# Kernel optimization log

Hardware: AMD Instinct MI355X
Metric: run time of the kernel (lower is better)

## Reference

```python
import jax, jax.numpy as jnp
import numpy as np

B, L, D = 1, 1024, 1024
NL = 4            # n_layers
N = 16            # d_state
DI = 2 * D        # d_inner (expand=2)
DTR = (D + 15) // 16  # dt_rank = ceil(d_model/16) = 64
K = 4             # depthwise conv kernel size
EPS = 1e-5


def setup_inputs() -> dict:
    key = jax.random.key(0)
    ks = jax.random.split(key, 8)
    s = lambda k, shp, sc: jax.random.normal(k, shp, jnp.float32) * sc
    x = s(ks[0], (B, L, D), 1.0)
    norm_w = jnp.ones((NL, D), jnp.float32)
    in_w = s(ks[1], (NL, 2 * DI, D), D ** -0.5)          # in_proj (no bias)
    conv_w = s(ks[2], (NL, DI, K), 0.5)                   # depthwise conv1d weight
    conv_b = s(ks[3], (NL, DI), 0.02)                     # conv1d bias
    xproj_w = s(ks[4], (NL, DTR + 2 * N, DI), DI ** -0.5) # x_proj (no bias)
    dt_w = s(ks[5], (NL, DI, DTR), DTR ** -0.5)           # dt_proj weight
    dt_b = jnp.full((NL, DI), 0.1, jnp.float32)           # dt_proj bias (positive-ish delta)
    A_log = jnp.log(jnp.tile(jnp.arange(1, N + 1, dtype=jnp.float32), (NL, DI, 1)))  # [NL, DI, N]
    D_skip = jnp.ones((NL, DI), jnp.float32)
    out_w = s(ks[6], (NL, D, DI), DI ** -0.5)             # out_proj (no bias)
    return dict(x=x, norm_w=norm_w, in_w=in_w, conv_w=conv_w, conv_b=conv_b,
                xproj_w=xproj_w, dt_w=dt_w, dt_b=dt_b, A_log=A_log,
                D_skip=D_skip, out_w=out_w)


def _rmsnorm(x, w):
    return x * jax.lax.rsqrt(jnp.mean(x * x, axis=-1, keepdims=True) + EPS) * w


def _causal_depthwise_conv(u, w, b):
    # u: [B, L, DI], w: [DI, K], b: [DI]; causal (left pad K-1)
    up = jnp.pad(u, ((0, 0), (K - 1, 0), (0, 0)))
    y = b
    for k in range(K):
        y = y + up[:, k:k + L, :] * w[:, k]
    return y


def _selective_scan(dA, dBu, C):
    # dA, dBu: [B, L, DI, N]; C: [B, L, N]
    def step(h, inp):
        a, bu, c = inp
        h = a * h + bu                       # [B, DI, N]
        y = jnp.einsum('bdn,bn->bd', h, c)   # [B, DI]
        return h, y
    h0 = jnp.zeros((dA.shape[0], DI, N), dA.dtype)
    _, ys = jax.lax.scan(step, h0, (dA.transpose(1, 0, 2, 3),
                                    dBu.transpose(1, 0, 2, 3),
                                    C.transpose(1, 0, 2)))
    return ys.transpose(1, 0, 2)             # [B, L, DI]


def _mamba_block(x, p):
    norm_w, in_w, conv_w, conv_b, xproj_w, dt_w, dt_b, A_log, D_skip, out_w = p
    xn = _rmsnorm(x, norm_w)
    xz = jnp.einsum('bld,ed->ble', xn, in_w)             # [B, L, 2*DI]
    u, z = jnp.split(xz, 2, axis=-1)
    u = jax.nn.silu(_causal_depthwise_conv(u, conv_w, conv_b))
    x_dbl = jnp.einsum('bld,ed->ble', u, xproj_w)        # [B, L, DTR+2N]
    dt_r, Bt, Ct = jnp.split(x_dbl, [DTR, DTR + N], axis=-1)
    delta = jax.nn.softplus(jnp.einsum('blr,dr->bld', dt_r, dt_w) + dt_b)  # [B, L, DI]
    A = -jnp.exp(A_log)                                  # [DI, N]
    dA = jnp.exp(delta[..., None] * A)                   # [B, L, DI, N]
    dBu = delta[..., None] * Bt[:, :, None, :] * u[..., None]
    y = _selective_scan(dA, dBu, Ct) + u * D_skip        # [B, L, DI]
    y = y * jax.nn.silu(z)
    return x + jnp.einsum('ble,de->bld', y, out_w)       # residual


def reference(x, norm_w, in_w, conv_w, conv_b, xproj_w, dt_w, dt_b, A_log, D_skip, out_w):
    params = (norm_w, in_w, conv_w, conv_b, xproj_w, dt_w, dt_b, A_log, D_skip, out_w)
    out, _ = jax.lax.scan(lambda h, p: (_mamba_block(h, p), None), x, params)
    return out
```

## Files before the change

### kernel.cpp

```cpp
#include <hip/hip_runtime.h>
#include <hip/hip_bf16.h>
#include <stdint.h>

#define L 1024
#define D 1024
#define NLAYER 4
#define NSTATE 16
#define DI 2048
#define DTR 64
#define KCONV 4
#define XD 96
#define NC 64
#define CT 16
#define KSPLIT 8

typedef __attribute__((ext_vector_type(8))) short short8;
typedef __attribute__((ext_vector_type(4))) float floatx4;

__device__ __forceinline__ float siluf(float x) { return x / (1.f + __expf(-x)); }

__device__ __forceinline__ unsigned short f2bf(float x) {
    __hip_bfloat16 b = __float2bfloat16(x);
    return *reinterpret_cast<unsigned short*>(&b);
}

#ifndef __has_builtin
#define __has_builtin(x) 0
#endif
#if __has_builtin(__builtin_amdgcn_global_load_lds)
#define HAVE_GLD 1
#define GLD(gp, lp) __builtin_amdgcn_global_load_lds(                                  \
    (const __attribute__((address_space(1))) void*)(gp),                               \
    (__attribute__((address_space(3))) void*)(lp), 16, 0, 0)
#endif

#define N_IN4  1048576
#define N_XP4  49152
#define N_DT4  32768
#define N_OUT4 524288
#define N_CVT4 (N_IN4 + N_XP4 + N_DT4 + N_OUT4)

__global__ __launch_bounds__(256) void cvt_layer_kernel(
    const float* __restrict__ in_w, const float* __restrict__ xp_w,
    const float* __restrict__ dt_w, const float* __restrict__ out_w,
    __hip_bfloat16* __restrict__ in_bf, __hip_bfloat16* __restrict__ xp_bf,
    __hip_bfloat16* __restrict__ dt_bf, __hip_bfloat16* __restrict__ out_bf) {
    int i = blockIdx.x * 256 + threadIdx.x;
    if (i >= N_CVT4) return;
    const float* src;
    __hip_bfloat16* dst;
    int off;
    if (i < N_IN4) { src = in_w; dst = in_bf; off = i; }
    else if (i < N_IN4 + N_XP4) { src = xp_w; dst = xp_bf; off = i - N_IN4; }
    else if (i < N_IN4 + N_XP4 + N_DT4) { src = dt_w; dst = dt_bf; off = i - N_IN4 - N_XP4; }
    else { src = out_w; dst = out_bf; off = i - N_IN4 - N_XP4 - N_DT4; }
    float4 v = ((const float4*)src)[off];
    ushort4 o;
    o.x = f2bf(v.x); o.y = f2bf(v.y); o.z = f2bf(v.z); o.w = f2bf(v.w);
    ((ushort4*)dst)[off] = o;
}

__global__ __launch_bounds__(256) void rmsnorm_kernel(const float* __restrict__ x,
                                                      const float* __restrict__ w,
                                                      __hip_bfloat16* __restrict__ out) {
    int row = blockIdx.x;
    const float* xr = x + (size_t)row * D;
    float v[4];
    float s = 0.f;
#pragma unroll
    for (int i = 0; i < 4; ++i) {
        v[i] = xr[threadIdx.x + i * 256];
        s += v[i] * v[i];
    }
#pragma unroll
    for (int off = 32; off > 0; off >>= 1) s += __shfl_xor(s, off, 64);
    __shared__ float red[4];
    int wave = threadIdx.x >> 6;
    if ((threadIdx.x & 63) == 0) red[wave] = s;
    __syncthreads();
    float tot = red[0] + red[1] + red[2] + red[3];
    float inv = rsqrtf(tot * (1.f / D) + 1e-5f);
#pragma unroll
    for (int i = 0; i < 4; ++i) {
        int c = threadIdx.x + i * 256;
        out[(size_t)row * D + c] = __float2bfloat16(v[i] * inv * w[c]);
    }
}

#define BM 128
#define BN 64
#define BK 32

template <int EPI>
__global__ __launch_bounds__(256, 2) void gemm_mfma(
    const __hip_bfloat16* __restrict__ A, int lda,
    const __hip_bfloat16* __restrict__ B, int ldb,
    float* __restrict__ C, int ldc, int Nvalid,
    int kchunk, long zstride,
    const float* __restrict__ bias, const float* __restrict__ resid) {
    __shared__ __align__(16) __hip_bfloat16 As[BM * BK];
    __shared__ __align__(16) __hip_bfloat16 Bs[BN * BK];
    int tid = threadIdx.x;
    int wave = tid >> 6, lane = tid & 63;
    int m0 = blockIdx.y * BM, n0 = blockIdx.x * BN;
    int k_lo = blockIdx.z * kchunk;
    int k_hi = k_lo + kchunk;
    C += (long)blockIdx.z * zstride;
    int wr = wave >> 1, wc = wave & 1;
    int srow = lane >> 2, scol = (lane & 3) * 8;
    int q = lane >> 4, r = lane & 15;

    floatx4 acc[4][2] = {};

    const __hip_bfloat16* gA = A + (long)(m0 + wave * 32 + srow) * lda + scol;
    const __hip_bfloat16* gB = B + (long)(n0 + wave * 16 + srow) * ldb + scol;
    __hip_bfloat16* lA0 = As + (wave * 32) * BK;
    __hip_bfloat16* lA1 = As + (wave * 32 + 16) * BK;
    __hip_bfloat16* lB  = Bs + (wave * 16) * BK;

    for (int k0 = k_lo; k0 < k_hi; k0 += BK) {
#ifdef HAVE_GLD
        GLD(gA + k0, lA0);
        GLD(gA + (long)16 * lda + k0, lA1);
        GLD(gB + k0, lB);
#else
        short8 a0 = *(const short8*)(gA + k0);
        short8 a1 = *(const short8*)(gA + (long)16 * lda + k0);
        short8 b0 = *(const short8*)(gB + k0);
        *(short8*)(lA0 + lane * 8) = a0;
        *(short8*)(lA1 + lane * 8) = a1;
        *(short8*)(lB + lane * 8) = b0;
#endif
        __syncthreads();
        const short* Ap = (const short*)As;
        const short* Bp = (const short*)Bs;
        short8 af[4], bfr[2];
#pragma unroll
        for (int i = 0; i < 4; ++i)
            af[i] = *(const short8*)(Ap + (wr * 64 + i * 16 + r) * BK + q * 8);
#pragma unroll
        for (int j = 0; j < 2; ++j)
            bfr[j] = *(const short8*)(Bp + (wc * 32 + j * 16 + r) * BK + q * 8);
#pragma unroll
        for (int i = 0; i < 4; ++i)
#pragma unroll
            for (int j = 0; j < 2; ++j)
                acc[i][j] = __builtin_amdgcn_mfma_f32_16x16x32_bf16(af[i], bfr[j], acc[i][j], 0, 0, 0);
        __syncthreads();
    }

#pragma unroll
    for (int i = 0; i < 4; ++i) {
        int mrow = m0 + wr * 64 + i * 16 + q * 4;
#pragma unroll
        for (int j = 0; j < 2; ++j) {
            int ncol = n0 + wc * 32 + j * 16 + r;
            if (ncol < Nvalid) {
#pragma unroll
                for (int rr = 0; rr < 4; ++rr) {
                    float v = acc[i][j][rr];
                    int m = mrow + rr;
                    if (EPI == 1) {
                        v += bias[ncol];
                        v = v > 20.f ? v : log1pf(__expf(v));
                    } else if (EPI == 2) {
                        v += resid[(long)m * ldc + ncol];
                    }
                    C[(long)m * ldc + ncol] = v;
                }
            }
        }
    }
}

__global__ __launch_bounds__(256) void conv_silu_kernel(const float* __restrict__ xz,
                                                        const float* __restrict__ cw,
                                                        const float* __restrict__ cb,
                                                        __hip_bfloat16* __restrict__ u) {
    int idx = blockIdx.x * 256 + threadIdx.x;
    int d = idx & (DI - 1);
    int t = idx >> 11;
    float acc = cb[d];
#pragma unroll
    for (int k = 0; k < KCONV; ++k) {
        int tk = t - (KCONV - 1) + k;
        if (tk >= 0) acc += xz[(size_t)tk * (2 * DI) + d] * cw[d * KCONV + k];
    }
    u[idx] = __float2bfloat16(siluf(acc));
}

__global__ __launch_bounds__(256) void xdbl_reduce_kernel(const float* __restrict__ part,
                                                          float* __restrict__ xdbl,
                                                          __hip_bfloat16* __restrict__ xdbl_bf) {
    int i = blockIdx.x * 256 + threadIdx.x;
    float s = 0.f;
#pragma unroll
    for (int sp = 0; sp < KSPLIT; ++sp) s += part[(long)sp * L * XD + i];
    xdbl[i] = s;
    xdbl_bf[i] = __float2bfloat16(s);
}

__global__ __launch_bounds__(256) void scanA_kernel(const float* __restrict__ delta,
                                                    const __hip_bfloat16* __restrict__ u,
                                                    const float* __restrict__ xdbl,
                                                    const float* __restrict__ Alog,
                                                    float* __restrict__ Ach,
                                                    float* __restrict__ Bch) {
    int d = blockIdx.x * 256 + threadIdx.x;
    int c = blockIdx.y;
    __shared__ __align__(16) float Bsh[CT * NSTATE];
    int tt0 = threadIdx.x >> 4, c0 = threadIdx.x & 15;
    Bsh[threadIdx.x] = xdbl[(size_t)(c * CT + tt0) * XD + DTR + c0];
    __syncthreads();

    float aval[NSTATE];
    const float4* Al4 = (const float4*)(Alog + (size_t)d * NSTATE);
#pragma unroll
    for (int n4 = 0; n4 < 4; ++n4) {
        float4 t = Al4[n4];
        aval[n4 * 4 + 0] = -__expf(t.x);
        aval[n4 * 4 + 1] = -__expf(t.y);
        aval[n4 * 4 + 2] = -__expf(t.z);
        aval[n4 * 4 + 3] = -__expf(t.w);
    }
    float h[NSTATE], ap[NSTATE];
#pragma unroll
    for (int n = 0; n < NSTATE; ++n) { h[n] = 0.f; ap[n] = 1.f; }

    for (int tt = 0; tt < CT; ++tt) {
        int t = c * CT + tt;
        float dl = delta[(size_t)t * DI + d];
        float uu = __bfloat162float(u[(size_t)t * DI + d]);
        float du = dl * uu;
        const float4* Bv = (const float4*)(Bsh + tt * NSTATE);
#pragma unroll
        for (int n4 = 0; n4 < 4; ++n4) {
            float4 b = Bv[n4];
            float bb[4] = {b.x, b.y, b.z, b.w};
#pragma unroll
            for (int k = 0; k < 4; ++k) {
                int n = n4 * 4 + k;
                float a = __expf(dl * aval[n]);
                h[n] = a * h[n] + du * bb[k];
                ap[n] *= a;
            }
        }
    }
    float4* Ao = (float4*)(Ach + ((size_t)c * DI + d) * NSTATE);
    float4* Bo = (float4*)(Bch + ((size_t)c * DI + d) * NSTATE);
#pragma unroll
    for (int n4 = 0; n4 < 4; ++n4) {
        Ao[n4] = make_float4(ap[n4 * 4], ap[n4 * 4 + 1], ap[n4 * 4 + 2], ap[n4 * 4 + 3]);
        Bo[n4] = make_float4(h[n4 * 4], h[n4 * 4 + 1], h[n4 * 4 + 2], h[n4 * 4 + 3]);
    }
}

__global__ __launch_bounds__(256) void scanB_kernel(float* __restrict__ Ach,
                                                    const float* __restrict__ Bch) {
    long i = blockIdx.x * 256 + threadIdx.x;
    const long S = (long)DI * NSTATE;
    float h = 0.f;
    for (int c = 0; c < NC; ++c) {
        float a = Ach[c * S + i];
        float b = Bch[c * S + i];
        Ach[c * S + i] = h;
        h = a * h + b;
    }
}

__global__ __launch_bounds__(256) void scanC_kernel(const float* __restrict__ delta,
                                                    const __hip_bfloat16* __restrict__ u,
                                                    const float* __restrict__ xdbl,
                                                    const float* __restrict__ Alog,
                                                    const float* __restrict__ Hin,
                                                    const float* __restrict__ xz,
                                                    const float* __restrict__ Dskip,
                                                    __hip_bfloat16* __restrict__ yg) {
    int d = blockIdx.x * 256 + threadIdx.x;
    int c = blockIdx.y;
    __shared__ __align__(16) float Bsh[CT * NSTATE];
    __shared__ __align__(16) float Csh[CT * NSTATE];
    int tt0 = threadIdx.x >> 4, c0 = threadIdx.x & 15;
    Bsh[threadIdx.x] = xdbl[(size_t)(c * CT + tt0) * XD + DTR + c0];
    Csh[threadIdx.x] = xdbl[(size_t)(c * CT + tt0) * XD + DTR + NSTATE + c0];
    __syncthreads();

    float aval[NSTATE];
    const float4* Al4 = (const float4*)(Alog + (size_t)d * NSTATE);
#pragma unroll
    for (int n4 = 0; n4 < 4; ++n4) {
        float4 t = Al4[n4];
        aval[n4 * 4 + 0] = -__expf(t.x);
        aval[n4 * 4 + 1] = -__expf(t.y);
        aval[n4 * 4 + 2] = -__expf(t.z);
        aval[n4 * 4 + 3] = -__expf(t.w);
    }
    float h[NSTATE];
    const float4* Hi = (const float4*)(Hin + ((size_t)c * DI + d) * NSTATE);
#pragma unroll
    for (int n4 = 0; n4 < 4; ++n4) {
        float4 t = Hi[n4];
        h[n4 * 4 + 0] = t.x; h[n4 * 4 + 1] = t.y; h[n4 * 4 + 2] = t.z; h[n4 * 4 + 3] = t.w;
    }
    float dsk = Dskip[d];

    for (int tt = 0; tt < CT; ++tt) {
        int t = c * CT + tt;
        float dl = delta[(size_t)t * DI + d];
        float uu = __bfloat162float(u[(size_t)t * DI + d]);
        float du = dl * uu;
        const float4* Bv = (const float4*)(Bsh + tt * NSTATE);
        const float4* Cv = (const float4*)(Csh + tt * NSTATE);
        float y = 0.f;
#pragma unroll
        for (int n4 = 0; n4 < 4; ++n4) {
            float4 b = Bv[n4];
            float4 cc = Cv[n4];
            float bb[4] = {b.x, b.y, b.z, b.w};
            float cv[4] = {cc.x, cc.y, cc.z, cc.w};
#pragma unroll
            for (int k = 0; k < 4; ++k) {
                int n = n4 * 4 + k;
                float a = __expf(dl * aval[n]);
                h[n] = a * h[n] + du * bb[k];
                y += h[n] * cv[k];
            }
        }
        float z = xz[(size_t)t * (2 * DI) + DI + d];
        yg[(size_t)t * DI + d] = __float2bfloat16((y + uu * dsk) * siluf(z));
    }
}

extern "C" void kernel_launch(void* const* d_in, const int* in_sizes, int n_in,
                              void* d_out, int out_size, void* d_ws, size_t ws_size,
                              hipStream_t stream) {
    const float* x      = (const float*)d_in[0];
    const float* norm_w = (const float*)d_in[1];
    const float* in_w   = (const float*)d_in[2];
    const float* conv_w = (const float*)d_in[3];
    const float* conv_b = (const float*)d_in[4];
    const float* xproj_w= (const float*)d_in[5];
    const float* dt_w   = (const float*)d_in[6];
    const float* dt_b   = (const float*)d_in[7];
    const float* A_log  = (const float*)d_in[8];
    const float* D_skip = (const float*)d_in[9];
    const float* out_w  = (const float*)d_in[10];
    float* out = (float*)d_out;

    uint8_t* wp = (uint8_t*)d_ws;
    auto alloc = [&](size_t bytes) {
        uint8_t* p = wp;
        wp += (bytes + 255) & ~(size_t)255;
        return p;
    };
    __hip_bfloat16* w_in_bf  = (__hip_bfloat16*)alloc((size_t)4096 * 1024 * 2);
    __hip_bfloat16* w_xp_bf  = (__hip_bfloat16*)alloc((size_t)128 * 2048 * 2);
    __hip_bfloat16* w_dt_bf  = (__hip_bfloat16*)alloc((size_t)2048 * 64 * 2);
    __hip_bfloat16* w_out_bf = (__hip_bfloat16*)alloc((size_t)1024 * 2048 * 2);
    __hip_bfloat16* xn_bf    = (__hip_bfloat16*)alloc((size_t)L * D * 2);
    float*          xz       = (float*)alloc((size_t)L * 2 * DI * 4);
    __hip_bfloat16* u_bf     = (__hip_bfloat16*)alloc((size_t)L * DI * 2);
    float*          xdbl     = (float*)alloc((size_t)L * XD * 4);
    __hip_bfloat16* xdbl_bf  = (__hip_bfloat16*)alloc((size_t)L * XD * 2);
    float*          part     = (float*)alloc((size_t)KSPLIT * L * XD * 4);
    float*          delta    = (float*)alloc((size_t)L * DI * 4);
    __hip_bfloat16* yg_bf    = (__hip_bfloat16*)alloc((size_t)L * DI * 2);
    float*          Ach      = (float*)alloc((size_t)NC * DI * NSTATE * 4);
    float*          Bch      = (float*)alloc((size_t)NC * DI * NSTATE * 4);

    for (int l = 0; l < NLAYER; ++l) {
        const float* xin = (l == 0) ? x : out;

        cvt_layer_kernel<<<(N_CVT4 + 255) / 256, 256, 0, stream>>>(
            in_w + (size_t)l * 4096 * 1024, xproj_w + (size_t)l * 96 * 2048,
            dt_w + (size_t)l * 2048 * 64, out_w + (size_t)l * 1024 * 2048,
            w_in_bf, w_xp_bf, w_dt_bf, w_out_bf);

        rmsnorm_kernel<<<L, 256, 0, stream>>>(xin, norm_w + (size_t)l * D, xn_bf);

        gemm_mfma<0><<<dim3(4096 / BN, L / BM, 1), 256, 0, stream>>>(
            xn_bf, D, w_in_bf, D, xz, 4096, 4096, D, 0, nullptr, nullptr);

        conv_silu_kernel<<<L * DI / 256, 256, 0, stream>>>(
            xz, conv_w + (size_t)l * DI * KCONV, conv_b + (size_t)l * DI, u_bf);

        gemm_mfma<0><<<dim3(2, L / BM, KSPLIT), 256, 0, stream>>>(
            u_bf, DI, w_xp_bf, DI, part, XD, XD, DI / KSPLIT, (long)L * XD, nullptr, nullptr);
        xdbl_reduce_kernel<<<(L * XD) / 256, 256, 0, stream>>>(part, xdbl, xdbl_bf);

        gemm_mfma<1><<<dim3(2048 / BN, L / BM, 1), 256, 0, stream>>>(
            xdbl_bf, XD, w_dt_bf, DTR, delta, DI, DI, DTR, 0,
            dt_b + (size_t)l * DI, nullptr);

        scanA_kernel<<<dim3(DI / 256, NC), 256, 0, stream>>>(
            delta, u_bf, xdbl, A_log + (size_t)l * DI * NSTATE, Ach, Bch);
        scanB_kernel<<<(DI * NSTATE) / 256, 256, 0, stream>>>(Ach, Bch);
        scanC_kernel<<<dim3(DI / 256, NC), 256, 0, stream>>>(
            delta, u_bf, xdbl, A_log + (size_t)l * DI * NSTATE, Ach, xz,
            D_skip + (size_t)l * DI, yg_bf);

        gemm_mfma<2><<<dim3(1024 / BN, L / BM, 1), 256, 0, stream>>>(
            yg_bf, DI, w_out_bf, DI, out, D, D, DI, 0, nullptr, xin);
    }
}
```

Baseline: 682.5 us.

## Fuse weight bf16 conversion into register-pipelined GEMMs and fuse residual with next RMSNorm

Drops the per-layer weight conversion kernel. The GEMMs now load fp32 weights directly, pack them to bf16 in registers, and use a register-prefetch pipeline (DIST=4) with double-buffered LDS and one barrier per k-step. The out-proj GEMM is split-K by two, and its reduction kernel also adds the residual and computes the next layer's RMSNorm. The x_proj output is split into a bf16 dt part and a compact fp32 B/C buffer for the scan. This trades the extra conversion pass and launches for twice the weight-read bandwidth inside the GEMMs and higher register pressure.

```diff
diff --git a/kernel.cpp b/kernel.cpp
--- a/kernel.cpp
+++ b/kernel.cpp
@@ -13,6 +13,8 @@
 #define NC 64
 #define CT 16
 #define KSPLIT 8
+#define BK 32
+#define DIST 4
 
 typedef __attribute__((ext_vector_type(8))) short short8;
 typedef __attribute__((ext_vector_type(4))) float floatx4;
@@ -24,41 +26,16 @@
     return *reinterpret_cast<unsigned short*>(&b);
 }
 
-#ifndef __has_builtin
-#define __has_builtin(x) 0
-#endif
-#if __has_builtin(__builtin_amdgcn_global_load_lds)
-#define HAVE_GLD 1
-#define GLD(gp, lp) __builtin_amdgcn_global_load_lds(                                  \
-    (const __attribute__((address_space(1))) void*)(gp),                               \
-    (__attribute__((address_space(3))) void*)(lp), 16, 0, 0)
-#endif
-
-#define N_IN4  1048576
-#define N_XP4  49152
-#define N_DT4  32768
-#define N_OUT4 524288
-#define N_CVT4 (N_IN4 + N_XP4 + N_DT4 + N_OUT4)
-
-__global__ __launch_bounds__(256) void cvt_layer_kernel(
-    const float* __restrict__ in_w, const float* __restrict__ xp_w,
-    const float* __restrict__ dt_w, const float* __restrict__ out_w,
-    __hip_bfloat16* __restrict__ in_bf, __hip_bfloat16* __restrict__ xp_bf,
-    __hip_bfloat16* __restrict__ dt_bf, __hip_bfloat16* __restrict__ out_bf) {
-    int i = blockIdx.x * 256 + threadIdx.x;
-    if (i >= N_CVT4) return;
-    const float* src;
-    __hip_bfloat16* dst;
-    int off;
-    if (i < N_IN4) { src = in_w; dst = in_bf; off = i; }
-    else if (i < N_IN4 + N_XP4) { src = xp_w; dst = xp_bf; off = i - N_IN4; }
-    else if (i < N_IN4 + N_XP4 + N_DT4) { src = dt_w; dst = dt_bf; off = i - N_IN4 - N_XP4; }
-    else { src = out_w; dst = out_bf; off = i - N_IN4 - N_XP4 - N_DT4; }
-    float4 v = ((const float4*)src)[off];
-    ushort4 o;
-    o.x = f2bf(v.x); o.y = f2bf(v.y); o.z = f2bf(v.z); o.w = f2bf(v.w);
-    ((ushort4*)dst)[off] = o;
-}
+__device__ __forceinline__ short8 pack8(floatx4 a, floatx4 b) {
+    short8 o;
+    o[0] = (short)f2bf(a.x); o[1] = (short)f2bf(a.y);
+    o[2] = (short)f2bf(a.z); o[3] = (short)f2bf(a.w);
+    o[4] = (short)f2bf(b.x); o[5] = (short)f2bf(b.y);
+    o[6] = (short)f2bf(b.z); o[7] = (short)f2bf(b.w);
+    return o;
+}
+
+#define BARRIER_NODRAIN() asm volatile("s_waitcnt lgkmcnt(0)\n\ts_barrier" ::: "memory")
 
 __global__ __launch_bounds__(256) void rmsnorm_kernel(const float* __restrict__ x,
                                                       const float* __restrict__ w,
@@ -87,24 +64,18 @@
     }
 }
 
-#define BM 128
-#define BN 64
-#define BK 32
-
-template <int EPI>
-__global__ __launch_bounds__(256, 2) void gemm_mfma(
+template <int EPI, int ITERS>
+__global__ __launch_bounds__(256, 2) void gemm_pipe(
     const __hip_bfloat16* __restrict__ A, int lda,
-    const __hip_bfloat16* __restrict__ B, int ldb,
+    const float* __restrict__ Bw, int ldb, int Brows,
     float* __restrict__ C, int ldc, int Nvalid,
-    int kchunk, long zstride,
-    const float* __restrict__ bias, const float* __restrict__ resid) {
-    __shared__ __align__(16) __hip_bfloat16 As[BM * BK];
-    __shared__ __align__(16) __hip_bfloat16 Bs[BN * BK];
+    long zstride, const float* __restrict__ bias) {
+    __shared__ __align__(16) __hip_bfloat16 As[2][128 * BK];
+    __shared__ __align__(16) __hip_bfloat16 Bs[2][64 * BK];
     int tid = threadIdx.x;
     int wave = tid >> 6, lane = tid & 63;
-    int m0 = blockIdx.y * BM, n0 = blockIdx.x * BN;
-    int k_lo = blockIdx.z * kchunk;
-    int k_hi = k_lo + kchunk;
+    int m0 = blockIdx.y * 128, n0 = blockIdx.x * 64;
+    int k_base = blockIdx.z * (ITERS * BK);
     C += (long)blockIdx.z * zstride;
     int wr = wave >> 1, wc = wave & 1;
     int srow = lane >> 2, scol = (lane & 3) * 8;
@@ -112,28 +83,44 @@
 
     floatx4 acc[4][2] = {};
 
-    const __hip_bfloat16* gA = A + (long)(m0 + wave * 32 + srow) * lda + scol;
-    const __hip_bfloat16* gB = B + (long)(n0 + wave * 16 + srow) * ldb + scol;
-    __hip_bfloat16* lA0 = As + (wave * 32) * BK;
-    __hip_bfloat16* lA1 = As + (wave * 32 + 16) * BK;
-    __hip_bfloat16* lB  = Bs + (wave * 16) * BK;
-
-    for (int k0 = k_lo; k0 < k_hi; k0 += BK) {
-#ifdef HAVE_GLD
-        GLD(gA + k0, lA0);
-        GLD(gA + (long)16 * lda + k0, lA1);
-        GLD(gB + k0, lB);
-#else
-        short8 a0 = *(const short8*)(gA + k0);
-        short8 a1 = *(const short8*)(gA + (long)16 * lda + k0);
-        short8 b0 = *(const short8*)(gB + k0);
-        *(short8*)(lA0 + lane * 8) = a0;
-        *(short8*)(lA1 + lane * 8) = a1;
-        *(short8*)(lB + lane * 8) = b0;
-#endif
-        __syncthreads();
-        const short* Ap = (const short*)As;
-        const short* Bp = (const short*)Bs;
+    const __hip_bfloat16* gA0 = A + (long)(m0 + wave * 32 + srow) * lda + scol + k_base;
+    const __hip_bfloat16* gA1 = gA0 + (long)16 * lda;
+    int bn = n0 + wave * 16 + srow;
+    const float* gB = Bw + (long)bn * ldb + scol + k_base;
+    bool bok = bn < Brows;
+
+    short8 qa0[DIST], qa1[DIST];
+    floatx4 qb0[DIST] = {}, qb1[DIST] = {};
+
+    auto ld = [&](int j) {
+        int k0 = j * BK;
+        int s = j & (DIST - 1);
+        qa0[s] = *(const short8*)(gA0 + k0);
+        qa1[s] = *(const short8*)(gA1 + k0);
+        if (bok) {
+            qb0[s] = *(const floatx4*)(gB + k0);
+            qb1[s] = *(const floatx4*)(gB + k0 + 4);
+        }
+    };
+    auto wrstage = [&](int j) {
+        int p = j & 1, s = j & (DIST - 1);
+        *(short8*)(&As[p][(wave * 32 + srow) * BK + scol]) = qa0[s];
+        *(short8*)(&As[p][(wave * 32 + 16 + srow) * BK + scol]) = qa1[s];
+        *(short8*)(&Bs[p][(wave * 16 + srow) * BK + scol]) = pack8(qb0[s], qb1[s]);
+    };
+
+#pragma unroll
+    for (int j = 0; j < DIST; ++j)
+        if (j < ITERS) ld(j);
+    wrstage(0);
+
+#pragma unroll
+    for (int k = 0; k < ITERS; ++k) {
+        BARRIER_NODRAIN();
+        if (k + DIST < ITERS) ld(k + DIST);
+        if (k + 1 < ITERS) wrstage(k + 1);
+        const short* Ap = (const short*)As[k & 1];
+        const short* Bp = (const short*)Bs[k & 1];
         short8 af[4], bfr[2];
 #pragma unroll
         for (int i = 0; i < 4; ++i)
@@ -146,7 +133,6 @@
 #pragma unroll
             for (int j = 0; j < 2; ++j)
                 acc[i][j] = __builtin_amdgcn_mfma_f32_16x16x32_bf16(af[i], bfr[j], acc[i][j], 0, 0, 0);
-        __syncthreads();
     }
 
 #pragma unroll
@@ -163,12 +149,45 @@
                     if (EPI == 1) {
                         v += bias[ncol];
                         v = v > 20.f ? v : log1pf(__expf(v));
-                    } else if (EPI == 2) {
-                        v += resid[(long)m * ldc + ncol];
                     }
                     C[(long)m * ldc + ncol] = v;
                 }
             }
+        }
+    }
+}
+
+template <bool NORM>
+__global__ __launch_bounds__(256) void reduce2_kernel(const float* __restrict__ part2,
+                                                      const float* __restrict__ xin,
+                                                      const float* __restrict__ nw,
+                                                      float* __restrict__ out,
+                                                      __hip_bfloat16* __restrict__ xn) {
+    int row = blockIdx.x;
+    const float* p0 = part2 + (size_t)row * D;
+    const float* p1 = p0 + (size_t)L * D;
+    const float* xr = xin + (size_t)row * D;
+    float v[4];
+    float ss = 0.f;
+#pragma unroll
+    for (int i = 0; i < 4; ++i) {
+        int c = threadIdx.x + i * 256;
+        v[i] = p0[c] + p1[c] + xr[c];
+        out[(size_t)row * D + c] = v[i];
+        ss += v[i] * v[i];
+    }
+    if (NORM) {
+#pragma unroll
+        for (int off = 32; off > 0; off >>= 1) ss += __shfl_xor(ss, off, 64);
+        __shared__ float red[4];
+        int wave = threadIdx.x >> 6;
+        if ((threadIdx.x & 63) == 0) red[wave] = ss;
+        __syncthreads();
+        float inv = rsqrtf((red[0] + red[1] + red[2] + red[3]) * (1.f / D) + 1e-5f);
+#pragma unroll
+        for (int i = 0; i < 4; ++i) {
+            int c = threadIdx.x + i * 256;
+            xn[(size_t)row * D + c] = __float2bfloat16(v[i] * inv * nw[c]);
         }
     }
 }
@@ -189,20 +208,21 @@
     u[idx] = __float2bfloat16(siluf(acc));
 }
 
-__global__ __launch_bounds__(256) void xdbl_reduce_kernel(const float* __restrict__ part,
-                                                          float* __restrict__ xdbl,
-                                                          __hip_bfloat16* __restrict__ xdbl_bf) {
+__global__ __launch_bounds__(256) void xred_kernel(const float* __restrict__ part,
+                                                   __hip_bfloat16* __restrict__ xdbl_bf,
+                                                   float* __restrict__ xdblBC) {
     int i = blockIdx.x * 256 + threadIdx.x;
+    int t = i / XD, col = i - t * XD;
     float s = 0.f;
 #pragma unroll
-    for (int sp = 0; sp < KSPLIT; ++sp) s += part[(long)sp * L * XD + i];
-    xdbl[i] = s;
-    xdbl_bf[i] = __float2bfloat16(s);
+    for (int sp = 0; sp < KSPLIT; ++sp) s += part[(size_t)sp * L * XD + i];
+    if (col < DTR) xdbl_bf[(size_t)t * DTR + col] = __float2bfloat16(s);
+    else xdblBC[(size_t)t * 32 + (col - DTR)] = s;
 }
 
 __global__ __launch_bounds__(256) void scanA_kernel(const float* __restrict__ delta,
                                                     const __hip_bfloat16* __restrict__ u,
-                                                    const float* __restrict__ xdbl,
+                                                    const float* __restrict__ xdblBC,
                                                     const float* __restrict__ Alog,
                                                     float* __restrict__ Ach,
                                                     float* __restrict__ Bch) {
@@ -210,7 +230,7 @@
     int c = blockIdx.y;
     __shared__ __align__(16) float Bsh[CT * NSTATE];
     int tt0 = threadIdx.x >> 4, c0 = threadIdx.x & 15;
-    Bsh[threadIdx.x] = xdbl[(size_t)(c * CT + tt0) * XD + DTR + c0];
+    Bsh[threadIdx.x] = xdblBC[(size_t)(c * CT + tt0) * 32 + c0];
     __syncthreads();
 
     float aval[NSTATE];
@@ -270,7 +290,7 @@
 
 __global__ __launch_bounds__(256) void scanC_kernel(const float* __restrict__ delta,
                                                     const __hip_bfloat16* __restrict__ u,
-                                                    const float* __restrict__ xdbl,
+                                                    const float* __restrict__ xdblBC,
                                                     const float* __restrict__ Alog,
                                                     const float* __restrict__ Hin,
                                                     const float* __restrict__ xz,
@@ -281,8 +301,8 @@
     __shared__ __align__(16) float Bsh[CT * NSTATE];
     __shared__ __align__(16) float Csh[CT * NSTATE];
     int tt0 = threadIdx.x >> 4, c0 = threadIdx.x & 15;
-    Bsh[threadIdx.x] = xdbl[(size_t)(c * CT + tt0) * XD + DTR + c0];
-    Csh[threadIdx.x] = xdbl[(size_t)(c * CT + tt0) * XD + DTR + NSTATE + c0];
+    Bsh[threadIdx.x] = xdblBC[(size_t)(c * CT + tt0) * 32 + c0];
+    Csh[threadIdx.x] = xdblBC[(size_t)(c * CT + tt0) * 32 + 16 + c0];
     __syncthreads();
 
     float aval[NSTATE];
@@ -353,53 +373,55 @@
         wp += (bytes + 255) & ~(size_t)255;
         return p;
     };
-    __hip_bfloat16* w_in_bf  = (__hip_bfloat16*)alloc((size_t)4096 * 1024 * 2);
-    __hip_bfloat16* w_xp_bf  = (__hip_bfloat16*)alloc((size_t)128 * 2048 * 2);
-    __hip_bfloat16* w_dt_bf  = (__hip_bfloat16*)alloc((size_t)2048 * 64 * 2);
-    __hip_bfloat16* w_out_bf = (__hip_bfloat16*)alloc((size_t)1024 * 2048 * 2);
-    __hip_bfloat16* xn_bf    = (__hip_bfloat16*)alloc((size_t)L * D * 2);
-    float*          xz       = (float*)alloc((size_t)L * 2 * DI * 4);
-    __hip_bfloat16* u_bf     = (__hip_bfloat16*)alloc((size_t)L * DI * 2);
-    float*          xdbl     = (float*)alloc((size_t)L * XD * 4);
-    __hip_bfloat16* xdbl_bf  = (__hip_bfloat16*)alloc((size_t)L * XD * 2);
-    float*          part     = (float*)alloc((size_t)KSPLIT * L * XD * 4);
-    float*          delta    = (float*)alloc((size_t)L * DI * 4);
-    __hip_bfloat16* yg_bf    = (__hip_bfloat16*)alloc((size_t)L * DI * 2);
-    float*          Ach      = (float*)alloc((size_t)NC * DI * NSTATE * 4);
-    float*          Bch      = (float*)alloc((size_t)NC * DI * NSTATE * 4);
+    __hip_bfloat16* xn_bf   = (__hip_bfloat16*)alloc((size_t)L * D * 2);
+    float*          xz      = (float*)alloc((size_t)L * 2 * DI * 4);
+    __hip_bfloat16* u_bf    = (__hip_bfloat16*)alloc((size_t)L * DI * 2);
+    float*          part    = (float*)alloc((size_t)KSPLIT * L * XD * 4);
+    __hip_bfloat16* xdbl_bf = (__hip_bfloat16*)alloc((size_t)L * DTR * 2);
+    float*          xdblBC  = (float*)alloc((size_t)L * 32 * 4);
+    float*          delta   = (float*)alloc((size_t)L * DI * 4);
+    __hip_bfloat16* yg_bf   = (__hip_bfloat16*)alloc((size_t)L * DI * 2);
+    float*          part2   = (float*)alloc((size_t)2 * L * D * 4);
+    float*          Ach     = (float*)alloc((size_t)NC * DI * NSTATE * 4);
+    float*          Bch     = (float*)alloc((size_t)NC * DI * NSTATE * 4);
+
+    rmsnorm_kernel<<<L, 256, 0, stream>>>(x, norm_w, xn_bf);
 
     for (int l = 0; l < NLAYER; ++l) {
         const float* xin = (l == 0) ? x : out;
 
-        cvt_layer_kernel<<<(N_CVT4 + 255) / 256, 256, 0, stream>>>(
-            in_w + (size_t)l * 4096 * 1024, xproj_w + (size_t)l * 96 * 2048,
-            dt_w + (size_t)l * 2048 * 64, out_w + (size_t)l * 1024 * 2048,
-            w_in_bf, w_xp_bf, w_dt_bf, w_out_bf);
-
-        rmsnorm_kernel<<<L, 256, 0, stream>>>(xin, norm_w + (size_t)l * D, xn_bf);
-
-        gemm_mfma<0><<<dim3(4096 / BN, L / BM, 1), 256, 0, stream>>>(
-            xn_bf, D, w_in_bf, D, xz, 4096, 4096, D, 0, nullptr, nullptr);
+        gemm_pipe<0, 32><<<dim3(4096 / 64, L / 128, 1), 256, 0, stream>>>(
+            xn_bf, D, in_w + (size_t)l * 4096 * 1024, D, 4096,
+            xz, 4096, 4096, 0, nullptr);
 
         conv_silu_kernel<<<L * DI / 256, 256, 0, stream>>>(
             xz, conv_w + (size_t)l * DI * KCONV, conv_b + (size_t)l * DI, u_bf);
 
-        gemm_mfma<0><<<dim3(2, L / BM, KSPLIT), 256, 0, stream>>>(
-            u_bf, DI, w_xp_bf, DI, part, XD, XD, DI / KSPLIT, (long)L * XD, nullptr, nullptr);
-        xdbl_reduce_kernel<<<(L * XD) / 256, 256, 0, stream>>>(part, xdbl, xdbl_bf);
-
-        gemm_mfma<1><<<dim3(2048 / BN, L / BM, 1), 256, 0, stream>>>(
-            xdbl_bf, XD, w_dt_bf, DTR, delta, DI, DI, DTR, 0,
-            dt_b + (size_t)l * DI, nullptr);
+        gemm_pipe<0, 8><<<dim3(2, L / 128, KSPLIT), 256, 0, stream>>>(
+            u_bf, DI, xproj_w + (size_t)l * 96 * 2048, DI, 96,
+            part, XD, XD, (long)L * XD, nullptr);
+        xred_kernel<<<(L * XD) / 256, 256, 0, stream>>>(part, xdbl_bf, xdblBC);
+
+        gemm_pipe<1, 2><<<dim3(2048 / 64, L / 128, 1), 256, 0, stream>>>(
+            xdbl_bf, DTR, dt_w + (size_t)l * 2048 * 64, DTR, 2048,
+            delta, DI, DI, 0, dt_b + (size_t)l * DI);
 
         scanA_kernel<<<dim3(DI / 256, NC), 256, 0, stream>>>(
-            delta, u_bf, xdbl, A_log + (size_t)l * DI * NSTATE, Ach, Bch);
+            delta, u_bf, xdblBC, A_log + (size_t)l * DI * NSTATE, Ach, Bch);
         scanB_kernel<<<(DI * NSTATE) / 256, 256, 0, stream>>>(Ach, Bch);
         scanC_kernel<<<dim3(DI / 256, NC), 256, 0, stream>>>(
-            delta, u_bf, xdbl, A_log + (size_t)l * DI * NSTATE, Ach, xz,
+            delta, u_bf, xdblBC, A_log + (size_t)l * DI * NSTATE, Ach, xz,
             D_skip + (size_t)l * DI, yg_bf);
 
-        gemm_mfma<2><<<dim3(1024 / BN, L / BM, 1), 256, 0, stream>>>(
-            yg_bf, DI, w_out_bf, DI, out, D, D, DI, 0, nullptr, xin);
-    }
-}
+        gemm_pipe<0, 32><<<dim3(1024 / 64, L / 128, 2), 256, 0, stream>>>(
+            yg_bf, DI, out_w + (size_t)l * 1024 * 2048, DI, 1024,
+            part2, D, D, (long)L * D, nullptr);
+
+        if (l < NLAYER - 1)
+            reduce2_kernel<true><<<L, 256, 0, stream>>>(
+                part2, xin, norm_w + (size_t)(l + 1) * D, out, xn_bf);
+        else
+            reduce2_kernel<false><<<L, 256, 0, stream>>>(
+                part2, xin, nullptr, out, nullptr);
+    }
+}
```

Result: faster. 601.6 us (-11.9%).
